# Performance work log

Hardware: AMD Instinct MI355X
Metric: run time of the kernel (lower is better)

## Reference

```python
import jax, jax.numpy as jnp
import numpy as np

N = 30000        # entities
R_EFF = 9        # 2*r+1 after enrich() with r=4
F_IN = 256       # insize
HID = 256        # hidden
NCLS = 32        # numcls
BASES = 16
E = 500000       # number of (enriched) triples / nonzeros


def setup_inputs() -> dict:
    key = jax.random.key(0)
    ks = jax.random.split(key, 8)
    features = jax.random.normal(ks[0], (N, F_IN), dtype=jnp.float32)
    # sparse vertical adjacency: entry at (rel*N + dst, src)
    ver_rows = jax.random.randint(ks[1], (E,), 0, R_EFF * N, dtype=jnp.int32)
    ver_cols = jax.random.randint(ks[2], (E,), 0, N, dtype=jnp.int32)
    # row-sum normalization (sum_sparse in the original): vals = 1 / row_degree
    deg = jax.ops.segment_sum(jnp.ones((E,), jnp.float32), ver_rows,
                              num_segments=R_EFF * N)
    ver_vals = 1.0 / deg[ver_rows]
    # xavier-uniform-ish params
    def xavier(k, shape):
        fan_in, fan_out = shape[-2], shape[-1]
        lim = jnp.sqrt(6.0 / (fan_in + fan_out)) * jnp.sqrt(2.0)  # relu gain
        return jax.random.uniform(k, shape, jnp.float32, -lim, lim)
    comps1 = xavier(ks[3], (R_EFF, BASES))
    bases1 = xavier(ks[4], (BASES, F_IN, HID))
    comps2 = xavier(ks[5], (R_EFF, BASES))
    bases2 = xavier(ks[6], (BASES, HID, NCLS))
    bias1 = jnp.zeros((HID,), jnp.float32)
    bias2 = jnp.zeros((NCLS,), jnp.float32)
    return {"features": features, "ver_vals": ver_vals,
            "comps1": comps1, "bases1": bases1,
            "comps2": comps2, "bases2": bases2,
            "bias1": bias1, "bias2": bias2,
            "ver_rows": ver_rows, "ver_cols": ver_cols}


def _spmm(vals, rows, cols, x, num_rows):
    # sparse [num_rows, n] @ x [n, d] -> [num_rows, d]
    msg = vals[:, None] * x[cols]          # (E, d) gather + scale
    return jax.ops.segment_sum(msg, rows, num_segments=num_rows)


def reference(features, ver_vals, comps1, bases1, comps2, bases2,
              bias1, bias2, ver_rows, ver_cols):
    n, f = features.shape
    r = comps1.shape[0]
    # layer 1: sparse aggregate, per-relation transform (basis decomp), sum over r
    h = _spmm(ver_vals, ver_rows, ver_cols, features, r * n)  # (r*n, f)
    h = h.reshape(r, n, f)
    w1 = jnp.einsum('rb,bfe->rfe', comps1, bases1)            # (r, f, hid)
    h = jnp.einsum('rnf,rfe->ne', h, w1)                      # bmm + sum over r
    h = jax.nn.relu(h + bias1)                                # (n, hid)
    # layer 2
    e = h.shape[1]
    h2 = _spmm(ver_vals, ver_rows, ver_cols, h, r * n).reshape(r, n, e)
    w2 = jnp.einsum('rb,bec->rec', comps2, bases2)            # (r, hid, ncls)
    out = jnp.einsum('rne,rec->nc', h2, w2) + bias2           # link_prediction=False
    return out
```

## Files before the change

### kernel.cpp

```cpp
#include <hip/hip_runtime.h>

typedef __attribute__((ext_vector_type(8))) short bf16x8;
typedef __attribute__((ext_vector_type(4))) float f32x4;

constexpr int NB = 16;
constexpr int REFF = 9;
constexpr int NXCD = 8;

__device__ __forceinline__ unsigned short f2bf(float f) {
  unsigned u = __float_as_uint(f);
  u += 0x7FFFu + ((u >> 16) & 1u);
  return (unsigned short)(u >> 16);
}
__device__ __forceinline__ float bf2f(short s) {
  return __uint_as_float(((unsigned)(unsigned short)s) << 16);
}
__device__ __forceinline__ float bflo(unsigned u) {
  return __uint_as_float(u << 16);
}
__device__ __forceinline__ float bfhi(unsigned u) {
  return __uint_as_float(u & 0xFFFF0000u);
}

__device__ __forceinline__ unsigned short pack_w_one(const float* __restrict__ comps,
                                                     const float* __restrict__ bases,
                                                     int idx, int NTI, int NTOT) {
  int j = idx & 7;
  int lane = (idx >> 3) & 63;
  int ni = (idx >> 9) % NTI;
  int t = (idx >> 9) / NTI;
  int ks = t & 7;
  int r = t >> 3;
  int k = ks * 32 + ((lane >> 4) << 3) + j;
  int n = ni * 16 + (lane & 15);
  float acc = 0.f;
#pragma unroll
  for (int b = 0; b < NB; ++b)
    acc += comps[r * NB + b] * bases[(size_t)b * 256 * NTOT + (size_t)k * NTOT + n];
  return f2bf(acc);
}

__global__ void hist_prep_kernel(const int* __restrict__ rows,
                                 int* __restrict__ deg1, int E,
                                 const float* __restrict__ features,
                                 unsigned short* __restrict__ Xbf,
                                 const float* __restrict__ comps1,
                                 const float* __restrict__ bases1,
                                 unsigned short* __restrict__ W1p,
                                 const float* __restrict__ comps2,
                                 const float* __restrict__ bases2,
                                 unsigned short* __restrict__ W2p, int N) {
  int idx = blockIdx.x * 256 + threadIdx.x;
  if (idx < E) atomicAdd(&deg1[rows[idx]], 1);
  const int n4 = N * 64;
  const int PW1 = REFF * 8 * 16 * 512;
  const int PW2 = REFF * 8 * 2 * 512;
  if (idx < n4) {
    float4 f = reinterpret_cast<const float4*>(features)[idx];
    ushort4 o;
    o.x = f2bf(f.x); o.y = f2bf(f.y); o.z = f2bf(f.z); o.w = f2bf(f.w);
    reinterpret_cast<ushort4*>(Xbf)[idx] = o;
  } else if (idx < n4 + PW1) {
    int i = idx - n4;
    W1p[i] = pack_w_one(comps1, bases1, i, 16, 256);
  } else if (idx < n4 + PW1 + PW2) {
    int i = idx - n4 - PW1;
    W2p[i] = pack_w_one(comps2, bases2, i, 2, 32);
  }
}

__global__ void scan1_kernel(const int* __restrict__ deg, int* __restrict__ bsum,
                             int NR) {
  __shared__ int s[256];
  int t = threadIdx.x;
  int base = blockIdx.x * 1024 + t * 4;
  int acc = 0;
#pragma unroll
  for (int q = 0; q < 4; ++q)
    if (base + q < NR) acc += deg[base + q];
  s[t] = acc;
  __syncthreads();
  for (int off = 128; off > 0; off >>= 1) {
    if (t < off) s[t] += s[t + off];
    __syncthreads();
  }
  if (t == 0) bsum[blockIdx.x] = s[0];
}

__global__ void scan23_kernel(const int* __restrict__ deg,
                              const int* __restrict__ bsum,
                              int* __restrict__ ptr, int NR, int E) {
  __shared__ int s[256];
  __shared__ int sbase;
  int t = threadIdx.x;
  int b = blockIdx.x;
  int part = 0;
  for (int i = t; i < b; i += 256) part += bsum[i];
  s[t] = part;
  __syncthreads();
  for (int off = 128; off > 0; off >>= 1) {
    if (t < off) s[t] += s[t + off];
    __syncthreads();
  }
  if (t == 0) sbase = s[0];
  __syncthreads();
  int base0 = sbase;
  __syncthreads();
  int base = b * 1024 + t * 4;
  int d[4];
#pragma unroll
  for (int q = 0; q < 4; ++q)
    d[q] = (base + q < NR) ? deg[base + q] : 0;
  int tsum = d[0] + d[1] + d[2] + d[3];
  s[t] = tsum;
  __syncthreads();
  for (int off = 1; off < 256; off <<= 1) {
    int x = (t >= off) ? s[t - off] : 0;
    __syncthreads();
    s[t] += x;
    __syncthreads();
  }
  int off0 = base0 + s[t] - tsum;
#pragma unroll
  for (int q = 0; q < 4; ++q) {
    if (base + q < NR) ptr[base + q] = off0;
    off0 += d[q];
  }
  if (b == 0 && t == 0) ptr[NR] = E;
}

__global__ void fill_kernel(const int* __restrict__ rows,
                            const int* __restrict__ cols,
                            int* __restrict__ deg1, const int* __restrict__ ptr1,
                            int* __restrict__ pay1, int E) {
  int e = blockIdx.x * 256 + threadIdx.x;
  if (e >= E) return;
  int g = rows[e];
  int o1 = atomicSub(&deg1[g], 1);
  pay1[ptr1[g] + o1 - 1] = cols[e];
}

__device__ __forceinline__ void gather_row_q(const int* __restrict__ pay,
                                             const int* __restrict__ ptr,
                                             const unsigned short* __restrict__ Xbf,
                                             char* lds, int node0, int N, int r,
                                             int qu, int l16) {
  const int rr = qu;
  const int node = node0 + rr;
  float acc[16];
#pragma unroll
  for (int j = 0; j < 16; ++j) acc[j] = 0.f;
  float s = 0.f;
  if (node < N) {
    int g = r * N + node;
    int p0 = ptr[g], p1 = ptr[g + 1];
    if (p1 > p0) s = 1.0f / (float)(p1 - p0);
    int cnext = 0;
    if (p0 < p1) cnext = pay[p0];
    for (int p = p0; p < p1; ++p) {
      int cc = cnext;
      if (p + 1 < p1) cnext = pay[p + 1];
      const unsigned short* xr = Xbf + (size_t)cc * 256 + l16 * 16;
      bf16x8 x0 = *reinterpret_cast<const bf16x8*>(xr);
      bf16x8 x1 = *reinterpret_cast<const bf16x8*>(xr + 8);
#pragma unroll
      for (int j = 0; j < 8; ++j) {
        acc[j] += bf2f(x0[j]);
        acc[8 + j] += bf2f(x1[j]);
      }
    }
  }
  uint4 o;
  o.x = (unsigned)f2bf(s * acc[0]) | ((unsigned)f2bf(s * acc[1]) << 16);
  o.y = (unsigned)f2bf(s * acc[2]) | ((unsigned)f2bf(s * acc[3]) << 16);
  o.z = (unsigned)f2bf(s * acc[4]) | ((unsigned)f2bf(s * acc[5]) << 16);
  o.w = (unsigned)f2bf(s * acc[6]) | ((unsigned)f2bf(s * acc[7]) << 16);
  *reinterpret_cast<uint4*>(lds + ((rr * 512 + l16 * 32) ^ ((rr & 7) << 4))) = o;
  o.x = (unsigned)f2bf(s * acc[8]) | ((unsigned)f2bf(s * acc[9]) << 16);
  o.y = (unsigned)f2bf(s * acc[10]) | ((unsigned)f2bf(s * acc[11]) << 16);
  o.z = (unsigned)f2bf(s * acc[12]) | ((unsigned)f2bf(s * acc[13]) << 16);
  o.w = (unsigned)f2bf(s * acc[14]) | ((unsigned)f2bf(s * acc[15]) << 16);
  *reinterpret_cast<uint4*>(lds + ((rr * 512 + l16 * 32 + 16) ^ ((rr & 7) << 4))) = o;
}

__global__ __launch_bounds__(512, 8)
void fused_l1(const int* __restrict__ pay1, const int* __restrict__ ptr1,
              const unsigned short* __restrict__ Xbf,
              const unsigned short* __restrict__ W1p,
              const float* __restrict__ bias1,
              const unsigned short* __restrict__ W2p,
              unsigned short* __restrict__ Y2, int N, int nwg) {
  __shared__ char smem[32 * 1024];
  char* bufA = smem;
  char* bufB = smem + 16 * 1024;
  const int tid = threadIdx.x;
  const int w = tid >> 6, lane = tid & 63;
  const int l15 = lane & 15, kg = lane >> 4;
  const int qu = tid >> 4, l16 = tid & 15;

  int bid;
  {
    int q = nwg / NXCD, rem = nwg % NXCD;
    int xcd = blockIdx.x % NXCD, idx = blockIdx.x / NXCD;
    bid = (xcd < rem ? xcd * (q + 1) : rem * (q + 1) + (xcd - rem) * q) + idx;
  }
  const int node0 = bid * 32;

  f32x4 acc[2][2];
#pragma unroll
  for (int mi = 0; mi < 2; ++mi)
#pragma unroll
    for (int ni = 0; ni < 2; ++ni) acc[mi][ni] = (f32x4)(0.f);

  gather_row_q(pay1, ptr1, Xbf, bufA, node0, N, 0, qu, l16);
  __syncthreads();

  for (int r = 0; r < REFF; ++r) {
    char* cur = (r & 1) ? bufB : bufA;
    if (r + 1 < REFF) {
      char* nxt = ((r + 1) & 1) ? bufB : bufA;
      gather_row_q(pay1, ptr1, Xbf, nxt, node0, N, r + 1, qu, l16);
    }
    __builtin_amdgcn_s_setprio(1);
#pragma unroll 2
    for (int ks = 0; ks < 8; ++ks) {
      bf16x8 a[2];
#pragma unroll
      for (int mi = 0; mi < 2; ++mi) {
        int row = mi * 16 + l15;
        int boff = (row * 512 + ks * 64 + (kg << 4)) ^ ((row & 7) << 4);
        a[mi] = *reinterpret_cast<const bf16x8*>(cur + boff);
      }
#pragma unroll
      for (int ni = 0; ni < 2; ++ni) {
        int niG = w * 2 + ni;
        bf16x8 b = *reinterpret_cast<const bf16x8*>(
            W1p + (((size_t)(r * 8 + ks) * 16 + niG) << 9) + lane * 8);
#pragma unroll
        for (int mi = 0; mi < 2; ++mi)
          acc[mi][ni] = __builtin_amdgcn_mfma_f32_16x16x32_bf16(a[mi], b,
                                                               acc[mi][ni], 0, 0, 0);
      }
    }
    __builtin_amdgcn_s_setprio(0);
    __syncthreads();
  }

#pragma unroll
  for (int mi = 0; mi < 2; ++mi) {
#pragma unroll
    for (int ni = 0; ni < 2; ++ni) {
      int col = (w * 2 + ni) * 16 + l15;
      float bb = bias1[col];
#pragma unroll
      for (int reg = 0; reg < 4; ++reg) {
        int row = mi * 16 + (kg << 2) + reg;
        float v = fmaxf(acc[mi][ni][reg] + bb, 0.f);
        int b = (row * 512 + col * 2) ^ ((row & 7) << 4);
        *reinterpret_cast<unsigned short*>(bufA + b) = f2bf(v);
      }
    }
  }
  __syncthreads();

  unsigned short* ys = reinterpret_cast<unsigned short*>(bufB) + w * 1024;
  for (int j = w; j < 18; j += 8) {
    int rp = j >> 1, mih = j & 1;
    f32x4 a2[2];
    a2[0] = (f32x4)(0.f);
    a2[1] = (f32x4)(0.f);
    __builtin_amdgcn_s_setprio(1);
#pragma unroll
    for (int ks = 0; ks < 8; ++ks) {
      bf16x8 b0 = *reinterpret_cast<const bf16x8*>(
          W2p + (((size_t)(rp * 8 + ks) * 2 + 0) << 9) + lane * 8);
      bf16x8 b1 = *reinterpret_cast<const bf16x8*>(
          W2p + (((size_t)(rp * 8 + ks) * 2 + 1) << 9) + lane * 8);
      int row = mih * 16 + l15;
      int boff = (row * 512 + ks * 64 + (kg << 4)) ^ ((row & 7) << 4);
      bf16x8 a = *reinterpret_cast<const bf16x8*>(bufA + boff);
      a2[0] = __builtin_amdgcn_mfma_f32_16x16x32_bf16(a, b0, a2[0], 0, 0, 0);
      a2[1] = __builtin_amdgcn_mfma_f32_16x16x32_bf16(a, b1, a2[1], 0, 0, 0);
    }
    __builtin_amdgcn_s_setprio(0);
#pragma unroll
    for (int reg = 0; reg < 4; ++reg) {
      int row16 = (kg << 2) + reg;
      ys[row16 * 32 + l15] = f2bf(a2[0][reg]);
      ys[row16 * 32 + 16 + l15] = f2bf(a2[1][reg]);
    }
    asm volatile("s_waitcnt lgkmcnt(0)" ::: "memory");
    {
      int row = lane >> 2;
      int chunk = lane & 3;
      uint4 v = *reinterpret_cast<const uint4*>(&ys[row * 32 + chunk * 8]);
      int grow = node0 + mih * 16 + row;
      if (grow < N)
        *reinterpret_cast<uint4*>(Y2 + (size_t)grow * (REFF * 32) + rp * 32 + chunk * 8) = v;
    }
  }
}

__global__ __launch_bounds__(512, 8)
void gather_out_kernel(const int* __restrict__ pay1,
                       const int* __restrict__ ptr1,
                       const unsigned short* __restrict__ Y2,
                       const float* __restrict__ bias2,
                       float* __restrict__ out, int N) {
  int wv = threadIdx.x >> 6;
  int lane = threadIdx.x & 63;
  int qw = lane >> 4, c = lane & 15;
  int n = blockIdx.x * 8 + wv;
  if (n >= N) return;
  float ax = 0.f, ay = 0.f;
  for (int r = qw; r < REFF; r += 4) {
    int g = r * N + n;
    int p0 = ptr1[g], p1 = ptr1[g + 1];
    if (p0 >= p1) continue;
    float v = 1.0f / (float)(p1 - p0);
    float sx = 0.f, sy = 0.f;
    int p = p0;
    for (; p + 2 <= p1; p += 2) {
      int c0 = pay1[p], c1 = pay1[p + 1];
      unsigned u0 = *reinterpret_cast<const unsigned*>(
          Y2 + (size_t)c0 * (REFF * 32) + r * 32 + c * 2);
      unsigned u1 = *reinterpret_cast<const unsigned*>(
          Y2 + (size_t)c1 * (REFF * 32) + r * 32 + c * 2);
      sx += bflo(u0) + bflo(u1);
      sy += bfhi(u0) + bfhi(u1);
    }
    if (p < p1) {
      int c0 = pay1[p];
      unsigned u0 = *reinterpret_cast<const unsigned*>(
          Y2 + (size_t)c0 * (REFF * 32) + r * 32 + c * 2);
      sx += bflo(u0);
      sy += bfhi(u0);
    }
    ax += v * sx;
    ay += v * sy;
  }
  ax += __shfl_xor(ax, 16); ay += __shfl_xor(ay, 16);
  ax += __shfl_xor(ax, 32); ay += __shfl_xor(ay, 32);
  if (lane < 16) {
    float2 o;
    o.x = ax + bias2[c * 2];
    o.y = ay + bias2[c * 2 + 1];
    reinterpret_cast<float2*>(out)[(size_t)n * 16 + c] = o;
  }
}

extern "C" void kernel_launch(void* const* d_in, const int* in_sizes, int n_in,
                              void* d_out, int out_size, void* d_ws, size_t ws_size,
                              hipStream_t stream) {
  const float* features = (const float*)d_in[0];
  const float* comps1   = (const float*)d_in[2];
  const float* bases1   = (const float*)d_in[3];
  const float* comps2   = (const float*)d_in[4];
  const float* bases2   = (const float*)d_in[5];
  const float* bias1    = (const float*)d_in[6];
  const float* bias2    = (const float*)d_in[7];
  const int* ver_rows   = (const int*)d_in[8];
  const int* ver_cols   = (const int*)d_in[9];

  const int N = in_sizes[0] / 256;
  const int E = in_sizes[1];
  const int NR = REFF * N;
  const int NT = (NR + 1023) / 1024;

  char* p = (char*)d_ws;
  unsigned short* Xbf = (unsigned short*)p; p += (size_t)N * 256 * 2;
  unsigned short* Y2  = (unsigned short*)p; p += (size_t)N * REFF * 32 * 2;
  unsigned short* W1p = (unsigned short*)p; p += (size_t)REFF * 65536 * 2;
  unsigned short* W2p = (unsigned short*)p; p += (size_t)REFF * 8192 * 2;
  int* ptr1 = (int*)p;  p += (size_t)(NR + 4) * 4;
  int* pay1 = (int*)p;  p += (size_t)E * 4;
  int* deg1 = (int*)p;  p += (size_t)NR * 4;
  int* bsum = (int*)p;  p += 512 * 4;

  hipMemsetAsync(deg1, 0, (size_t)NR * 4, stream);
  const int prep_total = N * 64 + REFF * 8 * 16 * 512 + REFF * 8 * 2 * 512;
  const int hp_grid = ((prep_total > E ? prep_total : E) + 255) / 256;
  hist_prep_kernel<<<hp_grid, 256, 0, stream>>>(ver_rows, deg1, E,
                                                features, Xbf,
                                                comps1, bases1, W1p,
                                                comps2, bases2, W2p, N);
  scan1_kernel<<<NT, 256, 0, stream>>>(deg1, bsum, NR);
  scan23_kernel<<<NT, 256, 0, stream>>>(deg1, bsum, ptr1, NR, E);
  fill_kernel<<<(E + 255) / 256, 256, 0, stream>>>(ver_rows, ver_cols,
                                                   deg1, ptr1, pay1, E);

  const int nwg = (N + 31) / 32;
  fused_l1<<<nwg, 512, 0, stream>>>(pay1, ptr1, Xbf, W1p, bias1,
                                    W2p, Y2, N, nwg);
  gather_out_kernel<<<(N + 7) / 8, 512, 0, stream>>>(pay1, ptr1, Y2, bias2,
                                                     (float*)d_out, N);
}
```

Baseline: 185.1 us.

## Replace LDS double-buffered gather with register prefetch of first neighbor rows

```diff
diff --git a/kernel.cpp b/kernel.cpp
--- a/kernel.cpp
+++ b/kernel.cpp
@@ -140,49 +140,6 @@
   pay1[ptr1[g] + o1 - 1] = cols[e];
 }
 
-__device__ __forceinline__ void gather_row_q(const int* __restrict__ pay,
-                                             const int* __restrict__ ptr,
-                                             const unsigned short* __restrict__ Xbf,
-                                             char* lds, int node0, int N, int r,
-                                             int qu, int l16) {
-  const int rr = qu;
-  const int node = node0 + rr;
-  float acc[16];
-#pragma unroll
-  for (int j = 0; j < 16; ++j) acc[j] = 0.f;
-  float s = 0.f;
-  if (node < N) {
-    int g = r * N + node;
-    int p0 = ptr[g], p1 = ptr[g + 1];
-    if (p1 > p0) s = 1.0f / (float)(p1 - p0);
-    int cnext = 0;
-    if (p0 < p1) cnext = pay[p0];
-    for (int p = p0; p < p1; ++p) {
-      int cc = cnext;
-      if (p + 1 < p1) cnext = pay[p + 1];
-      const unsigned short* xr = Xbf + (size_t)cc * 256 + l16 * 16;
-      bf16x8 x0 = *reinterpret_cast<const bf16x8*>(xr);
-      bf16x8 x1 = *reinterpret_cast<const bf16x8*>(xr + 8);
-#pragma unroll
-      for (int j = 0; j < 8; ++j) {
-        acc[j] += bf2f(x0[j]);
-        acc[8 + j] += bf2f(x1[j]);
-      }
-    }
-  }
-  uint4 o;
-  o.x = (unsigned)f2bf(s * acc[0]) | ((unsigned)f2bf(s * acc[1]) << 16);
-  o.y = (unsigned)f2bf(s * acc[2]) | ((unsigned)f2bf(s * acc[3]) << 16);
-  o.z = (unsigned)f2bf(s * acc[4]) | ((unsigned)f2bf(s * acc[5]) << 16);
-  o.w = (unsigned)f2bf(s * acc[6]) | ((unsigned)f2bf(s * acc[7]) << 16);
-  *reinterpret_cast<uint4*>(lds + ((rr * 512 + l16 * 32) ^ ((rr & 7) << 4))) = o;
-  o.x = (unsigned)f2bf(s * acc[8]) | ((unsigned)f2bf(s * acc[9]) << 16);
-  o.y = (unsigned)f2bf(s * acc[10]) | ((unsigned)f2bf(s * acc[11]) << 16);
-  o.z = (unsigned)f2bf(s * acc[12]) | ((unsigned)f2bf(s * acc[13]) << 16);
-  o.w = (unsigned)f2bf(s * acc[14]) | ((unsigned)f2bf(s * acc[15]) << 16);
-  *reinterpret_cast<uint4*>(lds + ((rr * 512 + l16 * 32 + 16) ^ ((rr & 7) << 4))) = o;
-}
-
 __global__ __launch_bounds__(512, 8)
 void fused_l1(const int* __restrict__ pay1, const int* __restrict__ ptr1,
               const unsigned short* __restrict__ Xbf,
@@ -191,8 +148,8 @@
               const unsigned short* __restrict__ W2p,
               unsigned short* __restrict__ Y2, int N, int nwg) {
   __shared__ char smem[32 * 1024];
-  char* bufA = smem;
-  char* bufB = smem + 16 * 1024;
+  char* tile = smem;
+  unsigned short* y2s = reinterpret_cast<unsigned short*>(smem + 16 * 1024);
   const int tid = threadIdx.x;
   const int w = tid >> 6, lane = tid & 63;
   const int l15 = lane & 15, kg = lane >> 4;
@@ -205,6 +162,8 @@
     bid = (xcd < rem ? xcd * (q + 1) : rem * (q + 1) + (xcd - rem) * q) + idx;
   }
   const int node0 = bid * 32;
+  const int node = node0 + qu;
+  const bool vnode = node < N;
 
   f32x4 acc[2][2];
 #pragma unroll
@@ -212,15 +171,86 @@
 #pragma unroll
     for (int ni = 0; ni < 2; ++ni) acc[mi][ni] = (f32x4)(0.f);
 
-  gather_row_q(pay1, ptr1, Xbf, bufA, node0, N, 0, qu, l16);
-  __syncthreads();
+  int pf_p0 = 0, pf_p1 = 0;
+  float pf_s = 0.f;
+  bf16x8 xa0, xa1, xb0, xb1;
+
+  if (vnode) {
+    int g = 0 * N + node;
+    pf_p0 = ptr1[g]; pf_p1 = ptr1[g + 1];
+    pf_s = (pf_p1 > pf_p0) ? 1.0f / (float)(pf_p1 - pf_p0) : 0.f;
+    if (pf_p0 < pf_p1) {
+      int c0 = pay1[pf_p0];
+      const unsigned short* xr = Xbf + (size_t)c0 * 256 + l16 * 16;
+      xa0 = *reinterpret_cast<const bf16x8*>(xr);
+      xa1 = *reinterpret_cast<const bf16x8*>(xr + 8);
+    }
+    if (pf_p0 + 1 < pf_p1) {
+      int c1 = pay1[pf_p0 + 1];
+      const unsigned short* xr = Xbf + (size_t)c1 * 256 + l16 * 16;
+      xb0 = *reinterpret_cast<const bf16x8*>(xr);
+      xb1 = *reinterpret_cast<const bf16x8*>(xr + 8);
+    }
+  }
 
   for (int r = 0; r < REFF; ++r) {
-    char* cur = (r & 1) ? bufB : bufA;
-    if (r + 1 < REFF) {
-      char* nxt = ((r + 1) & 1) ? bufB : bufA;
-      gather_row_q(pay1, ptr1, Xbf, nxt, node0, N, r + 1, qu, l16);
-    }
+    {
+      float a[16];
+#pragma unroll
+      for (int j = 0; j < 16; ++j) a[j] = 0.f;
+      if (vnode && pf_p1 > pf_p0) {
+#pragma unroll
+        for (int j = 0; j < 8; ++j) { a[j] += bf2f(xa0[j]); a[8 + j] += bf2f(xa1[j]); }
+        if (pf_p0 + 1 < pf_p1) {
+#pragma unroll
+          for (int j = 0; j < 8; ++j) { a[j] += bf2f(xb0[j]); a[8 + j] += bf2f(xb1[j]); }
+        }
+        int p = pf_p0 + 2;
+        int cn = 0;
+        if (p < pf_p1) cn = pay1[p];
+        for (; p < pf_p1; ++p) {
+          int cc = cn;
+          if (p + 1 < pf_p1) cn = pay1[p + 1];
+          const unsigned short* xr = Xbf + (size_t)cc * 256 + l16 * 16;
+          bf16x8 t0 = *reinterpret_cast<const bf16x8*>(xr);
+          bf16x8 t1 = *reinterpret_cast<const bf16x8*>(xr + 8);
+#pragma unroll
+          for (int j = 0; j < 8; ++j) { a[j] += bf2f(t0[j]); a[8 + j] += bf2f(t1[j]); }
+        }
+      }
+      float s = pf_s;
+      uint4 o;
+      o.x = (unsigned)f2bf(s * a[0]) | ((unsigned)f2bf(s * a[1]) << 16);
+      o.y = (unsigned)f2bf(s * a[2]) | ((unsigned)f2bf(s * a[3]) << 16);
+      o.z = (unsigned)f2bf(s * a[4]) | ((unsigned)f2bf(s * a[5]) << 16);
+      o.w = (unsigned)f2bf(s * a[6]) | ((unsigned)f2bf(s * a[7]) << 16);
+      *reinterpret_cast<uint4*>(tile + ((qu * 512 + l16 * 32) ^ ((qu & 7) << 4))) = o;
+      o.x = (unsigned)f2bf(s * a[8]) | ((unsigned)f2bf(s * a[9]) << 16);
+      o.y = (unsigned)f2bf(s * a[10]) | ((unsigned)f2bf(s * a[11]) << 16);
+      o.z = (unsigned)f2bf(s * a[12]) | ((unsigned)f2bf(s * a[13]) << 16);
+      o.w = (unsigned)f2bf(s * a[14]) | ((unsigned)f2bf(s * a[15]) << 16);
+      *reinterpret_cast<uint4*>(tile + ((qu * 512 + l16 * 32 + 16) ^ ((qu & 7) << 4))) = o;
+    }
+    __syncthreads();
+
+    if (r + 1 < REFF && vnode) {
+      int g = (r + 1) * N + node;
+      pf_p0 = ptr1[g]; pf_p1 = ptr1[g + 1];
+      pf_s = (pf_p1 > pf_p0) ? 1.0f / (float)(pf_p1 - pf_p0) : 0.f;
+      if (pf_p0 < pf_p1) {
+        int c0 = pay1[pf_p0];
+        const unsigned short* xr = Xbf + (size_t)c0 * 256 + l16 * 16;
+        xa0 = *reinterpret_cast<const bf16x8*>(xr);
+        xa1 = *reinterpret_cast<const bf16x8*>(xr + 8);
+      }
+      if (pf_p0 + 1 < pf_p1) {
+        int c1 = pay1[pf_p0 + 1];
+        const unsigned short* xr = Xbf + (size_t)c1 * 256 + l16 * 16;
+        xb0 = *reinterpret_cast<const bf16x8*>(xr);
+        xb1 = *reinterpret_cast<const bf16x8*>(xr + 8);
+      }
+    }
+
     __builtin_amdgcn_s_setprio(1);
 #pragma unroll 2
     for (int ks = 0; ks < 8; ++ks) {
@@ -229,7 +259,7 @@
       for (int mi = 0; mi < 2; ++mi) {
         int row = mi * 16 + l15;
         int boff = (row * 512 + ks * 64 + (kg << 4)) ^ ((row & 7) << 4);
-        a[mi] = *reinterpret_cast<const bf16x8*>(cur + boff);
+        a[mi] = *reinterpret_cast<const bf16x8*>(tile + boff);
       }
 #pragma unroll
       for (int ni = 0; ni < 2; ++ni) {
@@ -257,13 +287,13 @@
         int row = mi * 16 + (kg << 2) + reg;
         float v = fmaxf(acc[mi][ni][reg] + bb, 0.f);
         int b = (row * 512 + col * 2) ^ ((row & 7) << 4);
-        *reinterpret_cast<unsigned short*>(bufA + b) = f2bf(v);
-      }
-    }
-  }
-  __syncthreads();
-
-  unsigned short* ys = reinterpret_cast<unsigned short*>(bufB) + w * 1024;
+        *reinterpret_cast<unsigned short*>(tile + b) = f2bf(v);
+      }
+    }
+  }
+  __syncthreads();
+
+  unsigned short* ys = y2s + w * 1024;
   for (int j = w; j < 18; j += 8) {
     int rp = j >> 1, mih = j & 1;
     f32x4 a2[2];
@@ -278,7 +308,7 @@
           W2p + (((size_t)(rp * 8 + ks) * 2 + 1) << 9) + lane * 8);
       int row = mih * 16 + l15;
       int boff = (row * 512 + ks * 64 + (kg << 4)) ^ ((row & 7) << 4);
-      bf16x8 a = *reinterpret_cast<const bf16x8*>(bufA + boff);
+      bf16x8 a = *reinterpret_cast<const bf16x8*>(tile + boff);
       a2[0] = __builtin_amdgcn_mfma_f32_16x16x32_bf16(a, b0, a2[0], 0, 0, 0);
       a2[1] = __builtin_amdgcn_mfma_f32_16x16x32_bf16(a, b1, a2[1], 0, 0, 0);
     }
```

Result: slower. 222.2 us (+20.0%).
